# Kernel optimization log

Hardware: AMD Instinct MI355X
Metric: run time of the kernel (lower is better)

The kernel has to match this reference:

```python
import jax, jax.numpy as jnp
import numpy as np

B, H, W, C = 2, 64, 64, 512
EPS = 1e-3  # keras BatchNormalization default epsilon


def _bn(x, g, b, m, v):
    # inference-mode batch norm over the last axis
    return (x - m) * jax.lax.rsqrt(v + EPS) * g + b


def setup_inputs() -> dict:
    key = jax.random.key(0)
    ks = jax.random.split(key, 12)
    C2 = C // 2

    def he(k, shape, fan_in):
        return jax.random.normal(k, shape, jnp.float32) * np.float32(np.sqrt(2.0 / fan_in))

    def bn_params(k, n):
        k1, k2, k3, k4 = jax.random.split(k, 4)
        g = 1.0 + 0.1 * jax.random.normal(k1, (n,), jnp.float32)
        b = 0.1 * jax.random.normal(k2, (n,), jnp.float32)
        m = 0.1 * jax.random.normal(k3, (n,), jnp.float32)
        v = jax.random.uniform(k4, (n,), jnp.float32, 0.5, 1.5)
        return g, b, m, v

    g1, b1, m1, v1 = bn_params(ks[1], 1)
    g2, b2, m2, v2 = bn_params(ks[2], C2)
    g3, b3, m3, v3 = bn_params(ks[3], C2)
    g4, b4, m4, v4 = bn_params(ks[4], 1)
    g5, b5, m5, v5 = bn_params(ks[5], C)

    return {
        "x": jax.random.normal(ks[0], (B, H, W, C), jnp.float32),
        # edge_aggregation_func: Dense(1) over the 4-neighbor axis
        "w_ea": he(ks[6], (4, 1), 4), "b_ea": jnp.zeros((1,), jnp.float32),
        "g1": g1, "b1": b1, "m1": m1, "v1": v1,
        # vertex_update_func: Dense(C//2) over 2C features
        "w_vu": he(ks[7], (2 * C, C2), 2 * C), "b_vu": jnp.zeros((C2,), jnp.float32),
        "g2": g2, "b2": b2, "m2": m2, "v2": v2,
        # edge_update_func: Dense(C//2) over 2C features
        "w_eu": he(ks[8], (2 * C, C2), 2 * C), "b_eu": jnp.zeros((C2,), jnp.float32),
        "g3": g3, "b3": b3, "m3": m3, "v3": v3,
        # update_edge_reduce_func: Dense(1) over the 4-neighbor axis
        "w_er": he(ks[9], (4, 1), 4), "b_er": jnp.zeros((1,), jnp.float32),
        "g4": g4, "b4": b4, "m4": m4, "v4": v4,
        # final 1x1 conv (no bias): [C + C//2, C]
        "w_fc": he(ks[10], (C + C2, C), C + C2),
        "g5": g5, "b5": b5, "m5": m5, "v5": v5,
    }


def reference(x, w_ea, b_ea, g1, b1, m1, v1,
              w_vu, b_vu, g2, b2, m2, v2,
              w_eu, b_eu, g3, b3, m3, v3,
              w_er, b_er, g4, b4, m4, v4,
              w_fc, g5, b5, m5, v5):
    # 4-neighbor cyclic-shift edges: [B,H,W,C,4] (H+1, H-1, W+1, W-1 rolls)
    neigh = jnp.stack([
        jnp.roll(x, 1, axis=1), jnp.roll(x, -1, axis=1),
        jnp.roll(x, 1, axis=2), jnp.roll(x, -1, axis=2)], axis=-1)
    edge = neigh * x[..., None]                                   # [B,H,W,C,4]

    # edge aggregation: Dense(1) over neighbor axis + BN(1) + ReLU
    agg = jax.nn.relu(_bn(jnp.einsum('bhwcn,no->bhwco', edge, w_ea) + b_ea,
                          g1, b1, m1, v1))[..., 0]                # [B,H,W,C]

    # vertex update: Dense(C/2) on concat([vertex, agg]) + BN + ReLU
    cat_v = jnp.concatenate([x, agg], axis=-1)                    # [B,H,W,2C]
    uv = jax.nn.relu(_bn(cat_v @ w_vu + b_vu, g2, b2, m2, v2))    # [B,H,W,C/2]

    # edge update: Dense(C/2) on concat([vertex x4, edge]) along channel
    vert4 = jnp.broadcast_to(x[..., None], edge.shape)            # [B,H,W,C,4]
    cat_e = jnp.concatenate([vert4, edge], axis=3)                # [B,H,W,2C,4]
    ue = jax.nn.relu(_bn(jnp.einsum('bhwcn,cd->bhwnd', cat_e, w_eu) + b_eu,
                         g3, b3, m3, v3))                          # [B,H,W,4,C/2]

    # reduce updated edges over neighbor axis: Dense(1) + BN(1) + ReLU
    ur = jax.nn.relu(_bn(jnp.einsum('bhwnd,no->bhwdo', ue, w_er) + b_er,
                         g4, b4, m4, v4))[..., 0]                 # [B,H,W,C/2]

    update_feature = uv * ur                                      # [B,H,W,C/2]

    # final aggregation: 1x1 conv (no bias) on concat([x, update]) + BN + ReLU
    out = jax.nn.relu(_bn(jnp.concatenate([x, update_feature], axis=-1) @ w_fc,
                          g5, b5, m5, v5))                         # [B,H,W,C]
    return out
```

## Files before the change

### kernel.cpp

```cpp
#include <hip/hip_runtime.h>
#include <stdint.h>


typedef __attribute__((ext_vector_type(8))) short bf16x8;
typedef __attribute__((ext_vector_type(4))) float f32x4;

#define EPS_BN 1e-3f

__device__ __forceinline__ short f2bf(float f) {
    union { float f; unsigned u; } cv;
    cv.f = f;
    unsigned r = cv.u + 0x7fffu + ((cv.u >> 16) & 1u);
    return (short)(r >> 16);
}
__device__ __forceinline__ float bf2f(short s) {
    union { unsigned u; float f; } cv;
    cv.u = ((unsigned)(unsigned short)s) << 16;
    return cv.f;
}

#define GLOAD16(gsrc, ldst)                                                   \
    __builtin_amdgcn_global_load_lds(                                         \
        (const __attribute__((address_space(1))) void*)(gsrc),                \
        (__attribute__((address_space(3))) void*)(ldst), 16, 0, 0)


__device__ __forceinline__ void pack_one(const float* __restrict__ W, short* __restrict__ out,
                                         int K, int Ncol, int lb, int tid) {
    int i = lb * 256 + tid;
    int lane = i & 63, tile = i >> 6;
    int ktiles = K >> 5;
    int nt = tile / ktiles, kt = tile - nt * ktiles;
    int kbase = (kt << 5) + ((lane >> 4) << 3);
    int col = (nt << 4) + (lane & 15);
    bf16x8 v;
    #pragma unroll
    for (int j = 0; j < 8; ++j) v[j] = f2bf(W[(kbase + j) * Ncol + col]);
    ((bf16x8*)out)[(tile << 6) + lane] = v;
}

__global__ __launch_bounds__(256) void k_front(
    const float* __restrict__ x,
    const float* w_ea, const float* b_ea,
    const float* g1, const float* b1, const float* m1, const float* v1,
    const float* w_vu, const float* w_eu, const float* w_fc,
    const float* b_vu, const float* g2, const float* b2_, const float* m2, const float* v2,
    const float* b_eu, const float* g3, const float* b3, const float* m3, const float* v3,
    const float* w_er, const float* b_er,
    const float* g4, const float* b4, const float* m4, const float* v4,
    const float* g5, const float* b5, const float* m5, const float* v5,
    short* __restrict__ xb, short* __restrict__ agg,
    short* BpVu, short* BpEu, short* BpFc, float* P)
{
    int blk = blockIdx.x, t = threadIdx.x;
    if (blk >= 2048) {
        int b = blk - 2048;
        if (b < 128)      { pack_one(w_vu, BpVu, 1024, 256, b, t); }
        else if (b < 256) { pack_one(w_eu, BpEu, 1024, 256, b - 128, t); }
        else if (b < 448) { pack_one(w_fc, BpFc,  768, 512, b - 256, t); }
        else {
            for (int u = t; u < 512; u += 256) {
                float a5 = g5[u] * rsqrtf(v5[u] + EPS_BN);
                P[1032 + u] = a5;
                P[1544 + u] = b5[u] - m5[u] * a5;
            }
            {
                float a2 = g2[t] * rsqrtf(v2[t] + EPS_BN);
                P[8 + t]   = a2;
                P[264 + t] = (b_vu[t] - m2[t]) * a2 + b2_[t];
                float a3 = g3[t] * rsqrtf(v3[t] + EPS_BN);
                P[520 + t] = a3;
                P[776 + t] = (b_eu[t] - m3[t]) * a3 + b3[t];
            }
            if (t < 4) {
                P[2056 + t] = w_ea[t];
                P[2060 + t] = w_er[t];
            }
            if (t == 0) {
                float a4 = g4[0] * rsqrtf(v4[0] + EPS_BN);
                P[2] = a4;
                P[3] = (b_er[0] - m4[0]) * a4 + b4[0];
                float a1l = g1[0] * rsqrtf(v1[0] + EPS_BN);
                P[0] = a1l;
                P[1] = (b_ea[0] - m1[0]) * a1l + b1[0];
            }
        }
        return;
    }

    float a1 = g1[0] * rsqrtf(v1[0] + EPS_BN);
    float c1 = (b_ea[0] - m1[0]) * a1 + b1[0];
    float w0 = w_ea[0], w1 = w_ea[1], w2 = w_ea[2], w3 = w_ea[3];

    int idx = blk * 256 + t;
    int n = idx >> 6;
    int ci = idx & 63;
    int bh = n >> 6, h = bh & 63, w = n & 63;
    int bhb = bh & ~63;
    int rowU = ((bhb + ((h + 63) & 63)) << 6) + w;
    int rowD = ((bhb + ((h + 1) & 63)) << 6) + w;
    int rowL = (bh << 6) + ((w + 63) & 63);
    int rowR = (bh << 6) + ((w + 1) & 63);

    const f32x4* xv = (const f32x4*)x;
    int c4 = ci << 1;
    f32x4 vc[2], vU[2], vD[2], vL[2], vR[2];
    #pragma unroll
    for (int h2 = 0; h2 < 2; ++h2) {
        vc[h2] = xv[(n    << 7) + c4 + h2];
        vU[h2] = xv[(rowU << 7) + c4 + h2];
        vD[h2] = xv[(rowD << 7) + c4 + h2];
        vL[h2] = xv[(rowL << 7) + c4 + h2];
        vR[h2] = xv[(rowR << 7) + c4 + h2];
    }

    bf16x8 ob, xbv;
    #pragma unroll
    for (int h2 = 0; h2 < 2; ++h2) {
        #pragma unroll
        for (int j = 0; j < 4; ++j) {
            int e = h2 * 4 + j;
            float xc = vc[h2][j];
            float S = w0 * (xc * vU[h2][j]) + w1 * (xc * vD[h2][j])
                    + w2 * (xc * vL[h2][j]) + w3 * (xc * vR[h2][j]);
            ob[e]  = f2bf(fmaxf(fmaf(a1, S, c1), 0.f));
            xbv[e] = f2bf(xc);
        }
    }
    int o = (n << 6) + ci;
    ((bf16x8*)agg)[o] = ob;
    ((bf16x8*)xb)[o] = xbv;
}

#define MID_SRC(kc) ((type == 0) ? ((((kc) < 8) ? xb : agg) + sAoff + (((kc) & 7) << 6) + lcs) \
                                 : (xb + sAoff + ((kc) << 6) + lcs))

#define MID_GLOAD(slot, kc) GLOAD16(MID_SRC(kc), &sA[slot][wbase])

#define MID_LOAD(ga, na_, kc) do {                                            \
    ga = *(const bf16x8*)(xb + sAoff + ((kc) << 6) + lcs);                    \
    na_ = *(const bf16x8*)(xb + nAoff + ((kc) << 6) + lcs);                   \
} while (0)

#define MID_WRITE(slot, ga, na_) do {                                         \
    bf16x8 _va;                                                               \
    _Pragma("unroll") for (int _j = 0; _j < 8; ++_j)                          \
        _va[_j] = f2bf(bf2f(ga[_j]) * bf2f(na_[_j]));                         \
    ((bf16x8*)sA[slot])[t] = _va;                                             \
} while (0)

#define MID_COMPUTE(slot, kc) do {                                            \
    const short* _Lb = sA[slot];                                              \
    _Pragma("unroll") for (int _kt = 0; _kt < 2; ++_kt) {                     \
        bf16x8 _af[2];                                                        \
        _Pragma("unroll") for (int _mi = 0; _mi < 2; ++_mi) {                 \
            int _row = (_mi << 4) + (l & 15);                                 \
            int _lcolb = (_kt << 6) + ((l >> 4) << 4);                        \
            int _addr = (_row << 6) + ((_lcolb ^ ((_row & 7) << 4)) >> 1);    \
            _af[_mi] = *(const bf16x8*)(_Lb + _addr);                         \
        }                                                                     \
        int _kt32 = ktbase + ((kc) << 1) + _kt;                               \
        _Pragma("unroll") for (int _nf = 0; _nf < 4; ++_nf) {                 \
            bf16x8 _b = Bp[((((w << 2) + _nf) << 5) + _kt32) * 64 + l];       \
            _Pragma("unroll") for (int _mi = 0; _mi < 2; ++_mi)               \
                acc[_mi][_nf] = __builtin_amdgcn_mfma_f32_16x16x32_bf16(      \
                    _af[_mi], _b, acc[_mi][_nf], 0, 0, 0);                    \
        }                                                                     \
    }                                                                         \
} while (0)

__global__ __launch_bounds__(256) void k_gemm_mid(
    const short* __restrict__ xb, const short* __restrict__ agg,
    const short* __restrict__ BpVu, const short* __restrict__ BpEu,
    const float* __restrict__ P,
    short* __restrict__ uvb, short* __restrict__ tvb,
    short* __restrict__ teDb, short* __restrict__ teRb)
{
    __shared__ __align__(16) short sA[2][32 * 64];
    int t = threadIdx.x, l = t & 63, w = t >> 6;
    int type = blockIdx.x >> 8, rs = blockIdx.x & 255;
    int r0 = rs << 5;
    int dr = t >> 3, p8 = t & 7;
    int lcs = (p8 ^ (dr & 7)) << 3;
    int wbase = (t >> 6) << 9;

    int rA = r0 + dr;
    int nA = rA;
    if (type == 2) {
        int bh = rA >> 6;
        nA = (((bh & ~63) + (((bh & 63) + 1) & 63)) << 6) + (rA & 63);
    } else if (type == 3) {
        nA = (rA & ~63) + ((rA + 1) & 63);
    }
    int sAoff = rA << 9, nAoff = nA << 9;

    int nchunk = (type == 0) ? 16 : 8;
    const bf16x8* Bp = (type == 0) ? (const bf16x8*)BpVu : (const bf16x8*)BpEu;
    int ktbase = (type >= 2) ? 16 : 0;
    short* Out = (type == 0) ? uvb : (type == 1) ? tvb : (type == 2) ? teDb : teRb;

    f32x4 acc[2][4];
    #pragma unroll
    for (int mi = 0; mi < 2; ++mi)
        #pragma unroll
        for (int nf = 0; nf < 4; ++nf) acc[mi][nf] = (f32x4){0.f, 0.f, 0.f, 0.f};

    if (type <= 1) {
        MID_GLOAD(0, 0);
        for (int kc = 0; kc < nchunk; ++kc) {
            __syncthreads();
            if (kc + 1 < nchunk) MID_GLOAD((kc + 1) & 1, kc + 1);
            MID_COMPUTE(kc & 1, kc);
        }
    } else {
        bf16x8 gA, nAv, gB, nBv;
        MID_LOAD(gA, nAv, 0);
        MID_LOAD(gB, nBv, 1);
        for (int kc2 = 0; kc2 < nchunk; kc2 += 2) {
            MID_WRITE(0, gA, nAv);
            __syncthreads();
            if (kc2 + 2 < nchunk) MID_LOAD(gA, nAv, kc2 + 2);
            MID_COMPUTE(0, kc2);
            MID_WRITE(1, gB, nBv);
            __syncthreads();
            if (kc2 + 3 < nchunk) MID_LOAD(gB, nBv, kc2 + 3);
            MID_COMPUTE(1, kc2 + 1);
        }
    }

    #pragma unroll
    for (int nf = 0; nf < 4; ++nf) {
        int col = (w << 6) + (nf << 4) + (l & 15);
        float aa = P[8 + col], cc = P[264 + col];
        #pragma unroll
        for (int mi = 0; mi < 2; ++mi) {
            int rbase = r0 + (mi << 4) + ((l >> 4) << 2);
            #pragma unroll
            for (int j = 0; j < 4; ++j) {
                float v = acc[mi][nf][j];
                if (type == 0) v = fmaxf(fmaf(v, aa, cc), 0.f);
                Out[(rbase + j) * 256 + col] = f2bf(v);
            }
        }
    }
}

#define OUT_COMPUTE(Lb, kc) do {                                              \
    _Pragma("unroll") for (int _kt = 0; _kt < 2; ++_kt) {                     \
        bf16x8 _af[2];                                                        \
        _Pragma("unroll") for (int _mi = 0; _mi < 2; ++_mi) {                 \
            int _row = (_mi << 4) + (l & 15);                                 \
            int _lcolb = (_kt << 6) + ((l >> 4) << 4);                        \
            int _addr = (_row << 6) + ((_lcolb ^ ((_row & 7) << 4)) >> 1);    \
            _af[_mi] = *(const bf16x8*)((Lb) + _addr);                        \
        }                                                                     \
        _Pragma("unroll") for (int _nf = 0; _nf < 2; ++_nf) {                 \
            int _nt = (cq << 3) + (w << 1) + _nf;                             \
            bf16x8 _b = Bp[(_nt * 24 + ((kc) << 1) + _kt) * 64 + l];          \
            _Pragma("unroll") for (int _mi = 0; _mi < 2; ++_mi)               \
                acc[_mi][_nf] = __builtin_amdgcn_mfma_f32_16x16x32_bf16(      \
                    _af[_mi], _b, acc[_mi][_nf], 0, 0, 0);                    \
        }                                                                     \
    }                                                                         \
} while (0)

__global__ __launch_bounds__(256) void k_gemm_out(
    const short* __restrict__ xb,
    const short* __restrict__ tv, const short* __restrict__ teD,
    const short* __restrict__ teR, const short* __restrict__ uv,
    const short* __restrict__ BpFc, const float* __restrict__ P,
    float* __restrict__ out)
{
    __shared__ __align__(16) short sXb[2][32 * 64];
    __shared__ __align__(16) short updL[4][32 * 64];
    int t = threadIdx.x, l = t & 63, w = t >> 6;
    int cq = blockIdx.x & 3, rs = blockIdx.x >> 2;
    int r0 = rs << 5;
    const bf16x8* Bp = (const bf16x8*)BpFc;

    int dr = t >> 3, p8 = t & 7;
    int lcs = (p8 ^ (dr & 7)) << 3;
    int xrow = (r0 + dr) << 9;
    int wbase = (t >> 6) << 9;

    GLOAD16(xb + xrow + lcs, &sXb[0][wbase]);

    {
        int n = r0 + dr;
        int bh = n >> 6, h = bh & 63, ww = n & 63;
        int bhb = bh & ~63;
        int nUp = ((bhb + ((h + 63) & 63)) << 6) + ww;
        int nLf = (bh << 6) + ((ww + 63) & 63);
        float w0 = P[2060], w1 = P[2061], w2 = P[2062], w3 = P[2063];
        float a4 = P[2], c4 = P[3];
        #pragma unroll
        for (int q = 0; q < 4; ++q) {
            int lc = (q << 6) + lcs;
            bf16x8 vTv = *(const bf16x8*)(tv  + n   * 256 + lc);
            bf16x8 vD  = *(const bf16x8*)(teD + n   * 256 + lc);
            bf16x8 vDu = *(const bf16x8*)(teD + nUp * 256 + lc);
            bf16x8 vR  = *(const bf16x8*)(teR + n   * 256 + lc);
            bf16x8 vRl = *(const bf16x8*)(teR + nLf * 256 + lc);
            bf16x8 vUv = *(const bf16x8*)(uv  + n   * 256 + lc);
            f32x4 a3a = *(const f32x4*)&P[520 + lc], a3b = *(const f32x4*)&P[524 + lc];
            f32x4 c3a = *(const f32x4*)&P[776 + lc], c3b = *(const f32x4*)&P[780 + lc];
            bf16x8 o;
            #pragma unroll
            for (int j = 0; j < 8; ++j) {
                float a3 = (j < 4) ? a3a[j & 3] : a3b[j & 3];
                float c3 = (j < 4) ? c3a[j & 3] : c3b[j & 3];
                float tvv = bf2f(vTv[j]);
                float ueU = fmaxf(fmaf(a3, tvv + bf2f(vDu[j]), c3), 0.f);
                float ueD = fmaxf(fmaf(a3, tvv + bf2f(vD[j]),  c3), 0.f);
                float ueL = fmaxf(fmaf(a3, tvv + bf2f(vRl[j]), c3), 0.f);
                float ueR = fmaxf(fmaf(a3, tvv + bf2f(vR[j]),  c3), 0.f);
                float s = w0 * ueU + w1 * ueD + w2 * ueL + w3 * ueR;
                float ur = fmaxf(fmaf(a4, s, c4), 0.f);
                o[j] = f2bf(ur * bf2f(vUv[j]));
            }
            *(bf16x8*)&updL[q][(dr << 6) + (p8 << 3)] = o;
        }
    }

    f32x4 acc[2][2];
    #pragma unroll
    for (int mi = 0; mi < 2; ++mi)
        #pragma unroll
        for (int nf = 0; nf < 2; ++nf) acc[mi][nf] = (f32x4){0.f, 0.f, 0.f, 0.f};

    for (int kc = 0; kc < 8; ++kc) {
        __syncthreads();
        if (kc + 1 < 8)
            GLOAD16(xb + xrow + ((kc + 1) << 6) + lcs, &sXb[(kc + 1) & 1][wbase]);
        OUT_COMPUTE(sXb[kc & 1], kc);
    }
    #pragma unroll
    for (int ku = 0; ku < 4; ++ku) OUT_COMPUTE(updL[ku], 8 + ku);

    #pragma unroll
    for (int nf = 0; nf < 2; ++nf) {
        int col = (cq << 7) + (w << 5) + (nf << 4) + (l & 15);
        float a5 = P[1032 + col], c5 = P[1544 + col];
        #pragma unroll
        for (int mi = 0; mi < 2; ++mi) {
            int rbase = r0 + (mi << 4) + ((l >> 4) << 2);
            #pragma unroll
            for (int j = 0; j < 4; ++j) {
                out[(rbase + j) * 512 + col] = fmaxf(fmaf(acc[mi][nf][j], a5, c5), 0.f);
            }
        }
    }
}

extern "C" void kernel_launch(void* const* d_in, const int* in_sizes, int n_in,
                              void* d_out, int out_size, void* d_ws, size_t ws_size,
                              hipStream_t stream)
{
    const float* x    = (const float*)d_in[0];
    const float* w_ea = (const float*)d_in[1];
    const float* b_ea = (const float*)d_in[2];
    const float* g1   = (const float*)d_in[3];
    const float* b1   = (const float*)d_in[4];
    const float* m1   = (const float*)d_in[5];
    const float* v1   = (const float*)d_in[6];
    const float* w_vu = (const float*)d_in[7];
    const float* b_vu = (const float*)d_in[8];
    const float* g2   = (const float*)d_in[9];
    const float* b2   = (const float*)d_in[10];
    const float* m2   = (const float*)d_in[11];
    const float* v2   = (const float*)d_in[12];
    const float* w_eu = (const float*)d_in[13];
    const float* b_eu = (const float*)d_in[14];
    const float* g3   = (const float*)d_in[15];
    const float* b3   = (const float*)d_in[16];
    const float* m3   = (const float*)d_in[17];
    const float* v3   = (const float*)d_in[18];
    const float* w_er = (const float*)d_in[19];
    const float* b_er = (const float*)d_in[20];
    const float* g4   = (const float*)d_in[21];
    const float* b4   = (const float*)d_in[22];
    const float* m4   = (const float*)d_in[23];
    const float* v4   = (const float*)d_in[24];
    const float* w_fc = (const float*)d_in[25];
    const float* g5   = (const float*)d_in[26];
    const float* b5   = (const float*)d_in[27];
    const float* m5   = (const float*)d_in[28];
    const float* v5   = (const float*)d_in[29];

    char* ws = (char*)d_ws;
    float* P = (float*)ws;
    size_t off = 16384;
    short* BpVu = (short*)(ws + off); off += (size_t)1024 * 256 * 2;
    short* BpEu = (short*)(ws + off); off += (size_t)1024 * 256 * 2;
    short* BpFc = (short*)(ws + off); off += (size_t)768 * 512 * 2;
    short* xbb  = (short*)(ws + off); off += (size_t)8192 * 512 * 2;
    short* aggb = (short*)(ws + off); off += (size_t)8192 * 512 * 2;
    short* uvb  = (short*)(ws + off); off += (size_t)8192 * 256 * 2;
    short* tvb  = (short*)(ws + off); off += (size_t)8192 * 256 * 2;
    short* teDb = (short*)(ws + off); off += (size_t)8192 * 256 * 2;
    short* teRb = (short*)(ws + off); off += (size_t)8192 * 256 * 2;

    k_front<<<2497, 256, 0, stream>>>(x, w_ea, b_ea, g1, b1, m1, v1,
                                      w_vu, w_eu, w_fc,
                                      b_vu, g2, b2, m2, v2,
                                      b_eu, g3, b3, m3, v3,
                                      w_er, b_er, g4, b4, m4, v4,
                                      g5, b5, m5, v5,
                                      xbb, aggb, BpVu, BpEu, BpFc, P);
    k_gemm_mid<<<1024, 256, 0, stream>>>(xbb, aggb, BpVu, BpEu, P,
                                         uvb, tvb, teDb, teRb);
    k_gemm_out<<<1024, 256, 0, stream>>>(xbb, tvb, teDb, teRb, uvb, BpFc, P,
                                         (float*)d_out);
}
```

Measured before the change: 67.27 us.

## Enlarge GEMM row tiles to 64 and split output columns across blocks

Both GEMM kernels now process 64-row tiles instead of 32, with each wave computing a 4x2 grid of MFMA tiles. The mid kernel splits its 256 output columns into two halves across blocks, and the out kernel's grid drops to 512 blocks. The goal is to reuse each B-fragment load across more A rows and cut redundant global traffic for weights. The cost is more LDS and registers per block, which may lower occupancy, and fewer blocks in the out kernel.

Result: slower. 72.84 us (+8.3%).

```diff
diff --git a/kernel.cpp b/kernel.cpp
--- a/kernel.cpp
+++ b/kernel.cpp
@@ -135,34 +135,43 @@
 #define MID_SRC(kc) ((type == 0) ? ((((kc) < 8) ? xb : agg) + sAoff + (((kc) & 7) << 6) + lcs) \
                                  : (xb + sAoff + ((kc) << 6) + lcs))
 
-#define MID_GLOAD(slot, kc) GLOAD16(MID_SRC(kc), &sA[slot][wbase])
-
-#define MID_LOAD(ga, na_, kc) do {                                            \
-    ga = *(const bf16x8*)(xb + sAoff + ((kc) << 6) + lcs);                    \
+#define MID_GLOAD(slot, kc) do {                                              \
+    const short* _src = MID_SRC(kc);                                          \
+    GLOAD16(_src, &sA[slot][wbase]);                                          \
+    GLOAD16(_src + (32 << 9), &sA[slot][wbase + 2048]);                       \
+} while (0)
+
+#define MID_LOAD(ga, gb, na_, nb_, kc) do {                                   \
+    ga  = *(const bf16x8*)(xb + sAoff + ((kc) << 6) + lcs);                   \
+    gb  = *(const bf16x8*)(xb + sBoff + ((kc) << 6) + lcs);                   \
     na_ = *(const bf16x8*)(xb + nAoff + ((kc) << 6) + lcs);                   \
+    nb_ = *(const bf16x8*)(xb + nBoff + ((kc) << 6) + lcs);                   \
 } while (0)
 
-#define MID_WRITE(slot, ga, na_) do {                                         \
-    bf16x8 _va;                                                               \
-    _Pragma("unroll") for (int _j = 0; _j < 8; ++_j)                          \
+#define MID_WRITE(slot, ga, gb, na_, nb_) do {                                \
+    bf16x8 _va, _vb;                                                          \
+    _Pragma("unroll") for (int _j = 0; _j < 8; ++_j) {                        \
         _va[_j] = f2bf(bf2f(ga[_j]) * bf2f(na_[_j]));                         \
+        _vb[_j] = f2bf(bf2f(gb[_j]) * bf2f(nb_[_j]));                         \
+    }                                                                         \
     ((bf16x8*)sA[slot])[t] = _va;                                             \
+    ((bf16x8*)sA[slot])[256 + t] = _vb;                                       \
 } while (0)
 
 #define MID_COMPUTE(slot, kc) do {                                            \
     const short* _Lb = sA[slot];                                              \
     _Pragma("unroll") for (int _kt = 0; _kt < 2; ++_kt) {                     \
-        bf16x8 _af[2];                                                        \
-        _Pragma("unroll") for (int _mi = 0; _mi < 2; ++_mi) {                 \
+        bf16x8 _af[4];                                                        \
+        _Pragma("unroll") for (int _mi = 0; _mi < 4; ++_mi) {                 \
             int _row = (_mi << 4) + (l & 15);                                 \
             int _lcolb = (_kt << 6) + ((l >> 4) << 4);                        \
             int _addr = (_row << 6) + ((_lcolb ^ ((_row & 7) << 4)) >> 1);    \
             _af[_mi] = *(const bf16x8*)(_Lb + _addr);                         \
         }                                                                     \
         int _kt32 = ktbase + ((kc) << 1) + _kt;                               \
-        _Pragma("unroll") for (int _nf = 0; _nf < 4; ++_nf) {                 \
-            bf16x8 _b = Bp[((((w << 2) + _nf) << 5) + _kt32) * 64 + l];       \
-            _Pragma("unroll") for (int _mi = 0; _mi < 2; ++_mi)               \
+        _Pragma("unroll") for (int _nf = 0; _nf < 2; ++_nf) {                 \
+            bf16x8 _b = Bp[((nt0 + _nf) * 32 + _kt32) * 64 + l];              \
+            _Pragma("unroll") for (int _mi = 0; _mi < 4; ++_mi)               \
                 acc[_mi][_nf] = __builtin_amdgcn_mfma_f32_16x16x32_bf16(      \
                     _af[_mi], _b, acc[_mi][_nf], 0, 0, 0);                    \
         }                                                                     \
@@ -176,34 +185,38 @@
     short* __restrict__ uvb, short* __restrict__ tvb,
     short* __restrict__ teDb, short* __restrict__ teRb)
 {
-    __shared__ __align__(16) short sA[2][32 * 64];
+    __shared__ __align__(16) short sA[2][64 * 64];
     int t = threadIdx.x, l = t & 63, w = t >> 6;
-    int type = blockIdx.x >> 8, rs = blockIdx.x & 255;
-    int r0 = rs << 5;
+    int type = blockIdx.x >> 8, rem = blockIdx.x & 255;
+    int rs = rem >> 1, ch = rem & 1;
+    int r0 = rs << 6;
     int dr = t >> 3, p8 = t & 7;
     int lcs = (p8 ^ (dr & 7)) << 3;
     int wbase = (t >> 6) << 9;
-
-    int rA = r0 + dr;
-    int nA = rA;
+    int nt0 = (ch << 3) + (w << 1);
+
+    int rA = r0 + dr, rB = rA + 32;
+    int nA = rA, nB = rB;
     if (type == 2) {
-        int bh = rA >> 6;
-        nA = (((bh & ~63) + (((bh & 63) + 1) & 63)) << 6) + (rA & 63);
+        int bhA = rA >> 6, bhB = rB >> 6;
+        nA = (((bhA & ~63) + (((bhA & 63) + 1) & 63)) << 6) + (rA & 63);
+        nB = (((bhB & ~63) + (((bhB & 63) + 1) & 63)) << 6) + (rB & 63);
     } else if (type == 3) {
         nA = (rA & ~63) + ((rA + 1) & 63);
-    }
-    int sAoff = rA << 9, nAoff = nA << 9;
+        nB = (rB & ~63) + ((rB + 1) & 63);
+    }
+    int sAoff = rA << 9, sBoff = rB << 9, nAoff = nA << 9, nBoff = nB << 9;
 
     int nchunk = (type == 0) ? 16 : 8;
     const bf16x8* Bp = (type == 0) ? (const bf16x8*)BpVu : (const bf16x8*)BpEu;
     int ktbase = (type >= 2) ? 16 : 0;
     short* Out = (type == 0) ? uvb : (type == 1) ? tvb : (type == 2) ? teDb : teRb;
 
-    f32x4 acc[2][4];
-    #pragma unroll
-    for (int mi = 0; mi < 2; ++mi)
-        #pragma unroll
-        for (int nf = 0; nf < 4; ++nf) acc[mi][nf] = (f32x4){0.f, 0.f, 0.f, 0.f};
+    f32x4 acc[4][2];
+    #pragma unroll
+    for (int mi = 0; mi < 4; ++mi)
+        #pragma unroll
+        for (int nf = 0; nf < 2; ++nf) acc[mi][nf] = (f32x4){0.f, 0.f, 0.f, 0.f};
 
     if (type <= 1) {
         MID_GLOAD(0, 0);
@@ -213,27 +226,27 @@
             MID_COMPUTE(kc & 1, kc);
         }
     } else {
-        bf16x8 gA, nAv, gB, nBv;
-        MID_LOAD(gA, nAv, 0);
-        MID_LOAD(gB, nBv, 1);
+        bf16x8 g0a, g0b, n0a, n0b, g1a, g1b, n1a, n1b;
+        MID_LOAD(g0a, g0b, n0a, n0b, 0);
+        MID_LOAD(g1a, g1b, n1a, n1b, 1);
         for (int kc2 = 0; kc2 < nchunk; kc2 += 2) {
-            MID_WRITE(0, gA, nAv);
+            MID_WRITE(0, g0a, g0b, n0a, n0b);
             __syncthreads();
-            if (kc2 + 2 < nchunk) MID_LOAD(gA, nAv, kc2 + 2);
+            if (kc2 + 2 < nchunk) MID_LOAD(g0a, g0b, n0a, n0b, kc2 + 2);
             MID_COMPUTE(0, kc2);
-            MID_WRITE(1, gB, nBv);
+            MID_WRITE(1, g1a, g1b, n1a, n1b);
             __syncthreads();
-            if (kc2 + 3 < nchunk) MID_LOAD(gB, nBv, kc2 + 3);
+            if (kc2 + 3 < nchunk) MID_LOAD(g1a, g1b, n1a, n1b, kc2 + 3);
             MID_COMPUTE(1, kc2 + 1);
         }
     }
 
     #pragma unroll
-    for (int nf = 0; nf < 4; ++nf) {
-        int col = (w << 6) + (nf << 4) + (l & 15);
+    for (int nf = 0; nf < 2; ++nf) {
+        int col = (ch << 7) + (w << 5) + (nf << 4) + (l & 15);
         float aa = P[8 + col], cc = P[264 + col];
         #pragma unroll
-        for (int mi = 0; mi < 2; ++mi) {
+        for (int mi = 0; mi < 4; ++mi) {
             int rbase = r0 + (mi << 4) + ((l >> 4) << 2);
             #pragma unroll
             for (int j = 0; j < 4; ++j) {
@@ -247,17 +260,17 @@
 
 #define OUT_COMPUTE(Lb, kc) do {                                              \
     _Pragma("unroll") for (int _kt = 0; _kt < 2; ++_kt) {                     \
-        bf16x8 _af[2];                                                        \
-        _Pragma("unroll") for (int _mi = 0; _mi < 2; ++_mi) {                 \
+        bf16x8 _af[4];                                                        \
+        _Pragma("unroll") for (int _mi = 0; _mi < 4; ++_mi) {                 \
             int _row = (_mi << 4) + (l & 15);                                 \
             int _lcolb = (_kt << 6) + ((l >> 4) << 4);                        \
             int _addr = (_row << 6) + ((_lcolb ^ ((_row & 7) << 4)) >> 1);    \
             _af[_mi] = *(const bf16x8*)((Lb) + _addr);                        \
         }                                                                     \
+        int _kt32 = ((kc) << 1) + _kt;                                        \
         _Pragma("unroll") for (int _nf = 0; _nf < 2; ++_nf) {                 \
-            int _nt = (cq << 3) + (w << 1) + _nf;                             \
-            bf16x8 _b = Bp[(_nt * 24 + ((kc) << 1) + _kt) * 64 + l];          \
-            _Pragma("unroll") for (int _mi = 0; _mi < 2; ++_mi)               \
+            bf16x8 _b = Bp[((nt0 + _nf) * 24 + _kt32) * 64 + l];              \
+            _Pragma("unroll") for (int _mi = 0; _mi < 4; ++_mi)               \
                 acc[_mi][_nf] = __builtin_amdgcn_mfma_f32_16x16x32_bf16(      \
                     _af[_mi], _b, acc[_mi][_nf], 0, 0, 0);                    \
         }                                                                     \
@@ -271,67 +284,76 @@
     const short* __restrict__ BpFc, const float* __restrict__ P,
     float* __restrict__ out)
 {
-    __shared__ __align__(16) short sXb[2][32 * 64];
-    __shared__ __align__(16) short updL[4][32 * 64];
+    __shared__ __align__(16) short sXb[2][64 * 64];
+    __shared__ __align__(16) short updL[4][64 * 64];
     int t = threadIdx.x, l = t & 63, w = t >> 6;
     int cq = blockIdx.x & 3, rs = blockIdx.x >> 2;
-    int r0 = rs << 5;
+    int r0 = rs << 6;
     const bf16x8* Bp = (const bf16x8*)BpFc;
-
     int dr = t >> 3, p8 = t & 7;
     int lcs = (p8 ^ (dr & 7)) << 3;
-    int xrow = (r0 + dr) << 9;
     int wbase = (t >> 6) << 9;
-
-    GLOAD16(xb + xrow + lcs, &sXb[0][wbase]);
+    int nt0 = (cq << 3) + (w << 1);
+
+    int xrowA = (r0 + dr) << 9;
+
+    GLOAD16(xb + xrowA + lcs, &sXb[0][wbase]);
+    GLOAD16(xb + xrowA + (32 << 9) + lcs, &sXb[0][wbase + 2048]);
 
     {
-        int n = r0 + dr;
-        int bh = n >> 6, h = bh & 63, ww = n & 63;
-        int bhb = bh & ~63;
-        int nUp = ((bhb + ((h + 63) & 63)) << 6) + ww;
-        int nLf = (bh << 6) + ((ww + 63) & 63);
         float w0 = P[2060], w1 = P[2061], w2 = P[2062], w3 = P[2063];
         float a4 = P[2], c4 = P[3];
         #pragma unroll
-        for (int q = 0; q < 4; ++q) {
-            int lc = (q << 6) + lcs;
-            bf16x8 vTv = *(const bf16x8*)(tv  + n   * 256 + lc);
-            bf16x8 vD  = *(const bf16x8*)(teD + n   * 256 + lc);
-            bf16x8 vDu = *(const bf16x8*)(teD + nUp * 256 + lc);
-            bf16x8 vR  = *(const bf16x8*)(teR + n   * 256 + lc);
-            bf16x8 vRl = *(const bf16x8*)(teR + nLf * 256 + lc);
-            bf16x8 vUv = *(const bf16x8*)(uv  + n   * 256 + lc);
-            f32x4 a3a = *(const f32x4*)&P[520 + lc], a3b = *(const f32x4*)&P[524 + lc];
-            f32x4 c3a = *(const f32x4*)&P[776 + lc], c3b = *(const f32x4*)&P[780 + lc];
-            bf16x8 o;
+        for (int half = 0; half < 2; ++half) {
+            int row = dr + (half << 5);
+            int n = r0 + row;
+            int bh = n >> 6, h = bh & 63, ww = n & 63;
+            int bhb = bh & ~63;
+            int nUp = ((bhb + ((h + 63) & 63)) << 6) + ww;
+            int nLf = (bh << 6) + ((ww + 63) & 63);
             #pragma unroll
-            for (int j = 0; j < 8; ++j) {
-                float a3 = (j < 4) ? a3a[j & 3] : a3b[j & 3];
-                float c3 = (j < 4) ? c3a[j & 3] : c3b[j & 3];
-                float tvv = bf2f(vTv[j]);
-                float ueU = fmaxf(fmaf(a3, tvv + bf2f(vDu[j]), c3), 0.f);
-                float ueD = fmaxf(fmaf(a3, tvv + bf2f(vD[j]),  c3), 0.f);
-                float ueL = fmaxf(fmaf(a3, tvv + bf2f(vRl[j]), c3), 0.f);
-                float ueR = fmaxf(fmaf(a3, tvv + bf2f(vR[j]),  c3), 0.f);
-                float s = w0 * ueU + w1 * ueD + w2 * ueL + w3 * ueR;
-                float ur = fmaxf(fmaf(a4, s, c4), 0.f);
-                o[j] = f2bf(ur * bf2f(vUv[j]));
-            }
-            *(bf16x8*)&updL[q][(dr << 6) + (p8 << 3)] = o;
-        }
-    }
-
-    f32x4 acc[2][2];
-    #pragma unroll
-    for (int mi = 0; mi < 2; ++mi)
+            for (int q = 0; q < 4; ++q) {
+                int lc = (q << 6) + lcs;
+                bf16x8 vTv = *(const bf16x8*)(tv  + n   * 256 + lc);
+                bf16x8 vD  = *(const bf16x8*)(teD + n   * 256 + lc);
+                bf16x8 vDu = *(const bf16x8*)(teD + nUp * 256 + lc);
+                bf16x8 vR  = *(const bf16x8*)(teR + n   * 256 + lc);
+                bf16x8 vRl = *(const bf16x8*)(teR + nLf * 256 + lc);
+                bf16x8 vUv = *(const bf16x8*)(uv  + n   * 256 + lc);
+                f32x4 a3a = *(const f32x4*)&P[520 + lc], a3b = *(const f32x4*)&P[524 + lc];
+                f32x4 c3a = *(const f32x4*)&P[776 + lc], c3b = *(const f32x4*)&P[780 + lc];
+                bf16x8 o;
+                #pragma unroll
+                for (int j = 0; j < 8; ++j) {
+                    float a3 = (j < 4) ? a3a[j & 3] : a3b[j & 3];
+                    float c3 = (j < 4) ? c3a[j & 3] : c3b[j & 3];
+                    float tvv = bf2f(vTv[j]);
+                    float ueU = fmaxf(fmaf(a3, tvv + bf2f(vDu[j]), c3), 0.f);
+                    float ueD = fmaxf(fmaf(a3, tvv + bf2f(vD[j]),  c3), 0.f);
+                    float ueL = fmaxf(fmaf(a3, tvv + bf2f(vRl[j]), c3), 0.f);
+                    float ueR = fmaxf(fmaf(a3, tvv + bf2f(vR[j]),  c3), 0.f);
+                    float s = w0 * ueU + w1 * ueD + w2 * ueL + w3 * ueR;
+                    float ur = fmaxf(fmaf(a4, s, c4), 0.f);
+                    o[j] = f2bf(ur * bf2f(vUv[j]));
+                }
+                *(bf16x8*)&updL[q][(row << 6) + (p8 << 3)] = o;
+            }
+        }
+    }
+
+    f32x4 acc[4][2];
+    #pragma unroll
+    for (int mi = 0; mi < 4; ++mi)
         #pragma unroll
         for (int nf = 0; nf < 2; ++nf) acc[mi][nf] = (f32x4){0.f, 0.f, 0.f, 0.f};
 
     for (int kc = 0; kc < 8; ++kc) {
         __syncthreads();
-        if (kc + 1 < 8)
-            GLOAD16(xb + xrow + ((kc + 1) << 6) + lcs, &sXb[(kc + 1) & 1][wbase]);
+        if (kc + 1 < 8) {
+            GLOAD16(xb + xrowA + ((kc + 1) << 6) + lcs, &sXb[(kc + 1) & 1][wbase]);
+            GLOAD16(xb + xrowA + (32 << 9) + ((kc + 1) << 6) + lcs,
+                    &sXb[(kc + 1) & 1][wbase + 2048]);
+        }
         OUT_COMPUTE(sXb[kc & 1], kc);
     }
     #pragma unroll
@@ -342,7 +364,7 @@
         int col = (cq << 7) + (w << 5) + (nf << 4) + (l & 15);
         float a5 = P[1032 + col], c5 = P[1544 + col];
         #pragma unroll
-        for (int mi = 0; mi < 2; ++mi) {
+        for (int mi = 0; mi < 4; ++mi) {
             int rbase = r0 + (mi << 4) + ((l >> 4) << 2);
             #pragma unroll
             for (int j = 0; j < 4; ++j) {
@@ -409,6 +431,6 @@
                                       xbb, aggb, BpVu, BpEu, BpFc, P);
     k_gemm_mid<<<1024, 256, 0, stream>>>(xbb, aggb, BpVu, BpEu, P,
                                          uvb, tvb, teDb, teRb);
-    k_gemm_out<<<1024, 256, 0, stream>>>(xbb, tvb, teDb, teRb, uvb, BpFc, P,
-                                         (float*)d_out);
-}
+    k_gemm_out<<<512, 256, 0, stream>>>(xbb, tvb, teDb, teRb, uvb, BpFc, P,
+                                        (float*)d_out);
+}
```
